# Performance work log

Measured on AMD Instinct MI355X. Metric: run time of the kernel, lower is better.

Reference implementation:

```python
import jax, jax.numpy as jnp
import numpy as np
from jax.scipy.special import logsumexp

EPS = 0.1
MAX_ITER = 10
THRESH = 0.1


def setup_inputs() -> dict:
    key = jax.random.key(0)
    k1, k2 = jax.random.split(key)
    N, P, D = 16, 1024, 64
    y = jax.random.normal(k1, (N, P, D), dtype=jnp.float32)
    x = jax.random.normal(k2, (N, P, D), dtype=jnp.float32)
    return {"y": y, "x": x}


def reference(y, x):
    # Cost matrix |x_i - y_j|^2 summed over feature dim: (N, P1, P2)
    C = jnp.sum(jnp.abs(x[:, :, None, :] - y[:, None, :, :]) ** 2, axis=-1)
    N, P1, P2 = C.shape
    mu = jnp.full((N, P1), 1.0 / P1, dtype=C.dtype)
    nu = jnp.full((N, P2), 1.0 / P2, dtype=C.dtype)

    def M(u, v):
        # (-C + u_i + v_j) / eps
        return (-C + u[:, :, None] + v[:, None, :]) / EPS

    def body(carry, _):
        u, v, done = carry
        u_new = EPS * (jnp.log(mu + 1e-8) - logsumexp(M(u, v), axis=-1)) + u
        v_new = EPS * (jnp.log(nu + 1e-8) - logsumexp(M(u_new, v), axis=-2)) + v
        err = jnp.abs(u_new - u).sum(-1).mean()
        # emulate torch's early break: freeze updates once converged
        u2 = jnp.where(done, u, u_new)
        v2 = jnp.where(done, v, v_new)
        done2 = done | (err < THRESH)
        return (u2, v2, done2), None

    u0 = jnp.zeros_like(mu)
    v0 = jnp.zeros_like(nu)
    (u, v, _), _ = jax.lax.scan(body, (u0, v0, jnp.array(False)), None, length=MAX_ITER)
    pi = jnp.exp(M(u, v))  # transport plan (N, P1, P2)
    return pi
```

## Files before the change

### kernel.cpp

```cpp
#include <hip/hip_runtime.h>
#include <math.h>

#define NB 16
#define PP 1024
#define DD 64
#define MAX_ITER 10
#define RCH 16
#define NCH (PP / RCH)
#define NBLK (NB * NCH)

constexpr float EPSV    = 0.1f;
constexpr float SCALE_G = 20.0f;
constexpr float LOG2E   = 1.44269504088896340736f;
constexpr float LOG_MU  = -6.93146156597137f;
constexpr float THRESHV = 0.1f;

typedef short bf16x8 __attribute__((ext_vector_type(8)));
typedef float f32x16 __attribute__((ext_vector_type(16)));

__device__ __forceinline__ unsigned short f2bf(float f) {
  unsigned int u = __float_as_uint(f);
  return (unsigned short)((u + 0x7FFFu + ((u >> 16) & 1u)) >> 16);
}
__device__ __forceinline__ float bf2f(unsigned short h) {
  return __uint_as_float(((unsigned int)h) << 16);
}

__global__ __launch_bounds__(256) void prep_kernel(
    const float* __restrict__ x, const float* __restrict__ y,
    unsigned short* __restrict__ xh, unsigned short* __restrict__ xl,
    unsigned short* __restrict__ yh, unsigned short* __restrict__ yl,
    float* __restrict__ nxs, float* __restrict__ nys)
{
  const int sel = blockIdx.x >> 9;
  const int row = (blockIdx.x & 511) * 32 + (threadIdx.x >> 3);
  const int q   = threadIdx.x & 7;

  const float* src = sel ? y : x;
  unsigned short* H = sel ? yh : xh;
  unsigned short* L = sel ? yl : xl;
  float* N          = sel ? nys : nxs;

  const float* p = src + (size_t)row * DD + q * 8;
  float4 v0 = *(const float4*)(p);
  float4 v1 = *(const float4*)(p + 4);

  float f[8] = {v0.x, v0.y, v0.z, v0.w, v1.x, v1.y, v1.z, v1.w};
  float nrm = 0.f;
  unsigned short hb[8], lb[8];
  #pragma unroll
  for (int k = 0; k < 8; ++k) {
    nrm = fmaf(f[k], f[k], nrm);
    unsigned short h = f2bf(f[k]);
    float res = f[k] - bf2f(h);
    hb[k] = h; lb[k] = f2bf(res);
  }
  nrm += __shfl_xor(nrm, 1);
  nrm += __shfl_xor(nrm, 2);
  nrm += __shfl_xor(nrm, 4);
  if (q == 0) N[row] = 10.0f * nrm;

  uint4 ho, lo;
  ho.x = hb[0] | ((unsigned)hb[1] << 16); ho.y = hb[2] | ((unsigned)hb[3] << 16);
  ho.z = hb[4] | ((unsigned)hb[5] << 16); ho.w = hb[6] | ((unsigned)hb[7] << 16);
  lo.x = lb[0] | ((unsigned)lb[1] << 16); lo.y = lb[2] | ((unsigned)lb[3] << 16);
  lo.z = lb[4] | ((unsigned)lb[5] << 16); lo.w = lb[6] | ((unsigned)lb[7] << 16);
  *(uint4*)(H + (size_t)row * DD + q * 8) = ho;
  *(uint4*)(L + (size_t)row * DD + q * 8) = lo;
}

__global__ __launch_bounds__(256) void compute_c_mfma(
    const unsigned short* __restrict__ xh, const unsigned short* __restrict__ xl,
    const float* __restrict__ nxs,
    const unsigned short* __restrict__ yh, const unsigned short* __restrict__ yl,
    const float* __restrict__ nys,
    float* __restrict__ Cs)
{
  const int n   = blockIdx.x >> 8;
  const int ib  = (blockIdx.x >> 4) & 15;
  const int jb  = blockIdx.x & 15;
  const int tid = threadIdx.x;
  const int l   = tid & 63;
  const int w   = tid >> 6;
  const int ih  = w & 1, jh = w >> 1;

  __shared__ float nxv[64];
  if (tid < 64) nxv[tid] = nxs[n * PP + ib * 64 + tid];
  __syncthreads();

  const int jg  = n * PP + jb * 64 + 32 * jh + (l & 31);
  const float nyv = nys[jg];

  const int ko = 8 * (l >> 5);
  const size_t xrow = ((size_t)(n * PP + ib * 64 + 32 * ih + (l & 31))) * DD;
  const size_t yrow = ((size_t)jg) * DD;

  bf16x8 Xh0 = *(const bf16x8*)(xh + xrow + 0 * 16 + ko);
  bf16x8 Xh1 = *(const bf16x8*)(xh + xrow + 1 * 16 + ko);
  bf16x8 Xh2 = *(const bf16x8*)(xh + xrow + 2 * 16 + ko);
  bf16x8 Xh3 = *(const bf16x8*)(xh + xrow + 3 * 16 + ko);
  bf16x8 Xl0 = *(const bf16x8*)(xl + xrow + 0 * 16 + ko);
  bf16x8 Xl1 = *(const bf16x8*)(xl + xrow + 1 * 16 + ko);
  bf16x8 Xl2 = *(const bf16x8*)(xl + xrow + 2 * 16 + ko);
  bf16x8 Xl3 = *(const bf16x8*)(xl + xrow + 3 * 16 + ko);
  bf16x8 Yh0 = *(const bf16x8*)(yh + yrow + 0 * 16 + ko);
  bf16x8 Yh1 = *(const bf16x8*)(yh + yrow + 1 * 16 + ko);
  bf16x8 Yh2 = *(const bf16x8*)(yh + yrow + 2 * 16 + ko);
  bf16x8 Yh3 = *(const bf16x8*)(yh + yrow + 3 * 16 + ko);
  bf16x8 Yl0 = *(const bf16x8*)(yl + yrow + 0 * 16 + ko);
  bf16x8 Yl1 = *(const bf16x8*)(yl + yrow + 1 * 16 + ko);
  bf16x8 Yl2 = *(const bf16x8*)(yl + yrow + 2 * 16 + ko);
  bf16x8 Yl3 = *(const bf16x8*)(yl + yrow + 3 * 16 + ko);

  f32x16 acc;
  #pragma unroll
  for (int z = 0; z < 16; ++z) acc[z] = 0.f;
  acc = __builtin_amdgcn_mfma_f32_32x32x16_bf16(Xh0, Yh0, acc, 0, 0, 0);
  acc = __builtin_amdgcn_mfma_f32_32x32x16_bf16(Xh1, Yh1, acc, 0, 0, 0);
  acc = __builtin_amdgcn_mfma_f32_32x32x16_bf16(Xh2, Yh2, acc, 0, 0, 0);
  acc = __builtin_amdgcn_mfma_f32_32x32x16_bf16(Xh3, Yh3, acc, 0, 0, 0);
  acc = __builtin_amdgcn_mfma_f32_32x32x16_bf16(Xh0, Yl0, acc, 0, 0, 0);
  acc = __builtin_amdgcn_mfma_f32_32x32x16_bf16(Xh1, Yl1, acc, 0, 0, 0);
  acc = __builtin_amdgcn_mfma_f32_32x32x16_bf16(Xh2, Yl2, acc, 0, 0, 0);
  acc = __builtin_amdgcn_mfma_f32_32x32x16_bf16(Xh3, Yl3, acc, 0, 0, 0);
  acc = __builtin_amdgcn_mfma_f32_32x32x16_bf16(Xl0, Yh0, acc, 0, 0, 0);
  acc = __builtin_amdgcn_mfma_f32_32x32x16_bf16(Xl1, Yh1, acc, 0, 0, 0);
  acc = __builtin_amdgcn_mfma_f32_32x32x16_bf16(Xl2, Yh2, acc, 0, 0, 0);
  acc = __builtin_amdgcn_mfma_f32_32x32x16_bf16(Xl3, Yh3, acc, 0, 0, 0);

  const int irb  = 32 * ih + 4 * (l >> 5);
  const int jcol = jb * 64 + 32 * jh + (l & 31);
  #pragma unroll
  for (int r = 0; r < 16; ++r) {
    const int irel = irb + (r & 3) + 8 * (r >> 2);
    const size_t off = ((size_t)(n * PP + ib * 64 + irel)) * PP + jcol;
    Cs[off] = nxv[irel] + nyv - SCALE_G * acc[r];
  }
}

__global__ __launch_bounds__(256, 4) void iter_fused(
    const float* __restrict__ Cs, float* __restrict__ aG, const float* __restrict__ bG,
    float* __restrict__ pm, float* __restrict__ ps, float* __restrict__ errBlk,
    const int* __restrict__ doneFlags, int it)
{
  if (it > 0 && doneFlags[it - 1]) return;

  const int n   = blockIdx.x >> 6;
  const int rc  = blockIdx.x & (NCH - 1);
  const int tid = threadIdx.x;

  __shared__ float bb[PP];
  __shared__ float aArr[RCH];
  __shared__ float dsum[RCH];

  if (it == 0) {
    *(float4*)&bb[tid * 4] = make_float4(0.f, 0.f, 0.f, 0.f);
  } else {
    *(float4*)&bb[tid * 4] = *(const float4*)(bG + n * PP + tid * 4);
  }
  __syncthreads();

  const int r0  = tid >> 4;
  const int k   = tid & 15;
  const int row = n * PP + rc * RCH + r0;
  const float* crow = Cs + (size_t)row * PP + 4 * k;

  float4 tv[16];
  #pragma unroll
  for (int j = 0; j < 16; ++j) {
    float4 c4 = *(const float4*)(crow + 64 * j);
    float4 b4 = *(const float4*)&bb[4 * k + 64 * j];
    tv[j] = make_float4(b4.x - c4.x, b4.y - c4.y, b4.z - c4.z, b4.w - c4.w);
  }
  float m = -INFINITY;
  #pragma unroll
  for (int j = 0; j < 16; ++j)
    m = fmaxf(m, fmaxf(fmaxf(tv[j].x, tv[j].y), fmaxf(tv[j].z, tv[j].w)));
  #pragma unroll
  for (int mask = 8; mask; mask >>= 1) m = fmaxf(m, __shfl_xor(m, mask));

  float s = 0.f;
  #pragma unroll
  for (int j = 0; j < 16; ++j) {
    s += exp2f((tv[j].x - m) * LOG2E) + exp2f((tv[j].y - m) * LOG2E)
       + exp2f((tv[j].z - m) * LOG2E) + exp2f((tv[j].w - m) * LOG2E);
  }
  #pragma unroll
  for (int mask = 8; mask; mask >>= 1) s += __shfl_xor(s, mask);

  if (k == 0) {
    float aOld = (it == 0) ? 0.f : aG[row];
    float an = LOG_MU - (m + logf(s));
    aG[row]  = an;
    aArr[r0] = an;
    dsum[r0] = fabsf(an - aOld);
  }
  __syncthreads();
  if (tid == 0) {
    float e = 0.f;
    #pragma unroll
    for (int r = 0; r < RCH; ++r) e += dsum[r];
    errBlk[blockIdx.x] = e;
  }

  const int c0 = tid * 4;
  const float* cb = Cs + ((size_t)(n * PP + rc * RCH)) * PP + c0;

  float m0 = -INFINITY, m1 = -INFINITY, m2 = -INFINITY, m3 = -INFINITY;
  #pragma unroll
  for (int r = 0; r < RCH; ++r) {
    float ar = aArr[r];
    float4 c4 = *(const float4*)(cb + (size_t)r * PP);
    m0 = fmaxf(m0, ar - c4.x);
    m1 = fmaxf(m1, ar - c4.y);
    m2 = fmaxf(m2, ar - c4.z);
    m3 = fmaxf(m3, ar - c4.w);
  }
  float s0 = 0.f, s1 = 0.f, s2 = 0.f, s3 = 0.f;
  #pragma unroll
  for (int r = 0; r < RCH; ++r) {
    float ar = aArr[r];
    float4 c4 = *(const float4*)(cb + (size_t)r * PP);
    s0 += exp2f((ar - c4.x - m0) * LOG2E);
    s1 += exp2f((ar - c4.y - m1) * LOG2E);
    s2 += exp2f((ar - c4.z - m2) * LOG2E);
    s3 += exp2f((ar - c4.w - m3) * LOG2E);
  }
  size_t off = ((size_t)(n * NCH + rc)) * PP + c0;
  *(float4*)(pm + off) = make_float4(m0, m1, m2, m3);
  *(float4*)(ps + off) = make_float4(s0, s1, s2, s3);
}

__global__ __launch_bounds__(256) void v_combine(
    const float* __restrict__ pm, const float* __restrict__ ps,
    float* __restrict__ bG, const float* __restrict__ errBlk,
    int* __restrict__ doneFlags, int it)
{
  if (it > 0 && doneFlags[it - 1]) {
    if (blockIdx.x == 0 && threadIdx.x == 0) doneFlags[it] = 1;
    return;
  }
  const int col = blockIdx.x * 256 + threadIdx.x;
  const int n = col >> 10, j = col & (PP - 1);
  const float* pmn = pm + (size_t)n * NCH * PP + j;
  const float* psn = ps + (size_t)n * NCH * PP + j;

  float m = -INFINITY, s = 0.f;
  #pragma unroll 8
  for (int c = 0; c < NCH; ++c) {
    float mc = pmn[(size_t)c * PP];
    float sc = psn[(size_t)c * PP];
    float mn = fmaxf(m, mc);
    s = fmaf(s, exp2f((m - mn) * LOG2E), sc * exp2f((mc - mn) * LOG2E));
    m = mn;
  }
  bG[col] = LOG_MU - (m + logf(s));

  if (blockIdx.x == 0) {
    __shared__ float red[4];
    float loc = 0.f;
    for (int t = threadIdx.x; t < NBLK; t += 256) loc += errBlk[t];
    #pragma unroll
    for (int off = 32; off > 0; off >>= 1) loc += __shfl_xor(loc, off);
    if ((threadIdx.x & 63) == 0) red[threadIdx.x >> 6] = loc;
    __syncthreads();
    if (threadIdx.x == 0) {
      float tot = red[0] + red[1] + red[2] + red[3];
      float err = tot * (EPSV / (float)NB);
      doneFlags[it] = (err < THRESHV) ? 1 : 0;
    }
  }
}

__global__ __launch_bounds__(256) void pi_kernel(
    float* __restrict__ Cs, const float* __restrict__ a, const float* __restrict__ b)
{
  const int lane = threadIdx.x & 63;
  const int row  = (blockIdx.x << 2) + (threadIdx.x >> 6);
  const int n    = row >> 10;
  const float ai = a[row];
  float* crow = Cs + (size_t)row * PP;
  const float* bn = b + n * PP;
  #pragma unroll
  for (int kk = 0; kk < 4; ++kk) {
    float4 c4 = *(const float4*)(crow + lane * 4 + kk * 256);
    float4 b4 = *(const float4*)(bn   + lane * 4 + kk * 256);
    float4 r;
    r.x = exp2f((ai + b4.x - c4.x) * LOG2E);
    r.y = exp2f((ai + b4.y - c4.y) * LOG2E);
    r.z = exp2f((ai + b4.z - c4.z) * LOG2E);
    r.w = exp2f((ai + b4.w - c4.w) * LOG2E);
    *(float4*)(crow + lane * 4 + kk * 256) = r;
  }
}

extern "C" void kernel_launch(void* const* d_in, const int* in_sizes, int n_in,
                              void* d_out, int out_size, void* d_ws, size_t ws_size,
                              hipStream_t stream)
{
  const float* y = (const float*)d_in[0];
  const float* x = (const float*)d_in[1];

  float* Cs = (float*)d_out;

  const size_t NE = (size_t)NB * PP * DD;
  unsigned short* xh = (unsigned short*)d_ws;
  unsigned short* xl = xh + NE;
  unsigned short* yh = xl + NE;
  unsigned short* yl = yh + NE;
  float* pm = (float*)d_ws;
  float* ps = pm + (size_t)NB * NCH * PP;

  float* tail   = (float*)((char*)d_ws + 4 * NE * sizeof(unsigned short));
  float* nxs    = tail;
  float* nys    = nxs + NB * PP;
  float* aGl    = nys + NB * PP;
  float* bGl    = aGl + NB * PP;
  float* errBlk = bGl + NB * PP;
  int*   doneFl = (int*)(errBlk + NBLK);

  prep_kernel<<<1024, 256, 0, stream>>>(x, y, xh, xl, yh, yl, nxs, nys);
  compute_c_mfma<<<4096, 256, 0, stream>>>(xh, xl, nxs, yh, yl, nys, Cs);
  for (int it = 0; it < MAX_ITER; ++it) {
    iter_fused<<<NBLK, 256, 0, stream>>>(Cs, aGl, bGl, pm, ps, errBlk, doneFl, it);
    v_combine<<<NB * PP / 256, 256, 0, stream>>>(pm, ps, bGl, errBlk, doneFl, it);
  }
  pi_kernel<<<NB * PP / 4, 256, 0, stream>>>(Cs, aGl, bGl);
}
```

Measured before the change: 378.6 us.

## Recompute cost tiles with MFMA in row logsumexp and use column-stripe v update

```diff
diff --git a/kernel.cpp b/kernel.cpp
--- a/kernel.cpp
+++ b/kernel.cpp
@@ -5,9 +5,6 @@
 #define PP 1024
 #define DD 64
 #define MAX_ITER 10
-#define RCH 16
-#define NCH (PP / RCH)
-#define NBLK (NB * NCH)
 
 constexpr float EPSV    = 0.1f;
 constexpr float SCALE_G = 20.0f;
@@ -138,136 +135,205 @@
   }
 }
 
-__global__ __launch_bounds__(256, 4) void iter_fused(
-    const float* __restrict__ Cs, float* __restrict__ aG, const float* __restrict__ bG,
-    float* __restrict__ pm, float* __restrict__ ps, float* __restrict__ errBlk,
-    const int* __restrict__ doneFlags, int it)
-{
-  if (it > 0 && doneFlags[it - 1]) return;
-
-  const int n   = blockIdx.x >> 6;
-  const int rc  = blockIdx.x & (NCH - 1);
-  const int tid = threadIdx.x;
-
-  __shared__ float bb[PP];
-  __shared__ float aArr[RCH];
-  __shared__ float dsum[RCH];
-
-  if (it == 0) {
-    *(float4*)&bb[tid * 4] = make_float4(0.f, 0.f, 0.f, 0.f);
-  } else {
-    *(float4*)&bb[tid * 4] = *(const float4*)(bG + n * PP + tid * 4);
-  }
-  __syncthreads();
-
-  const int r0  = tid >> 4;
-  const int k   = tid & 15;
-  const int row = n * PP + rc * RCH + r0;
-  const float* crow = Cs + (size_t)row * PP + 4 * k;
-
-  float4 tv[16];
-  #pragma unroll
-  for (int j = 0; j < 16; ++j) {
-    float4 c4 = *(const float4*)(crow + 64 * j);
-    float4 b4 = *(const float4*)&bb[4 * k + 64 * j];
-    tv[j] = make_float4(b4.x - c4.x, b4.y - c4.y, b4.z - c4.z, b4.w - c4.w);
-  }
+__global__ __launch_bounds__(256) void u_mfma(
+    const unsigned short* __restrict__ yh, const unsigned short* __restrict__ yl,
+    const float* __restrict__ nys,
+    const unsigned short* __restrict__ xh, const unsigned short* __restrict__ xl,
+    const float* __restrict__ nxs,
+    const float* __restrict__ bG, float* __restrict__ aG,
+    float* __restrict__ errBlk, const int* __restrict__ doneFl, int it)
+{
+  if (it > 0 && doneFl[it - 1]) return;
+
+  const int n     = blockIdx.x >> 5;
+  const int itile = blockIdx.x & 31;
+  const int tid   = threadIdx.x;
+  const int l     = tid & 63;
+  const int w     = tid >> 6;
+
+  __shared__ float bt[PP];
+  __shared__ float mred[4][32];
+  __shared__ float sred[4][32];
+
+  {
+    float4 nv = *(const float4*)(nys + n * PP + tid * 4);
+    float4 b4 = make_float4(0.f, 0.f, 0.f, 0.f);
+    if (it > 0) b4 = *(const float4*)(bG + n * PP + tid * 4);
+    bt[tid * 4 + 0] = b4.x - nv.x; bt[tid * 4 + 1] = b4.y - nv.y;
+    bt[tid * 4 + 2] = b4.z - nv.z; bt[tid * 4 + 3] = b4.w - nv.w;
+  }
+  __syncthreads();
+
+  const size_t brow = ((size_t)(n * PP + itile * 32 + (l & 31))) * DD;
+  const int ko = 8 * (l >> 5);
+  bf16x8 Bh0 = *(const bf16x8*)(xh + brow + 0 * 16 + ko);
+  bf16x8 Bh1 = *(const bf16x8*)(xh + brow + 1 * 16 + ko);
+  bf16x8 Bh2 = *(const bf16x8*)(xh + brow + 2 * 16 + ko);
+  bf16x8 Bh3 = *(const bf16x8*)(xh + brow + 3 * 16 + ko);
+  bf16x8 Bl0 = *(const bf16x8*)(xl + brow + 0 * 16 + ko);
+  bf16x8 Bl1 = *(const bf16x8*)(xl + brow + 1 * 16 + ko);
+  bf16x8 Bl2 = *(const bf16x8*)(xl + brow + 2 * 16 + ko);
+  bf16x8 Bl3 = *(const bf16x8*)(xl + brow + 3 * 16 + ko);
+
+  float M = -INFINITY;
+  for (int jt = 0; jt < 8; ++jt) {
+    const int jrow0 = w * 256 + jt * 32;
+    const size_t arow = ((size_t)(n * PP + jrow0 + (l & 31))) * DD;
+    bf16x8 Ah0 = *(const bf16x8*)(yh + arow + 0 * 16 + ko);
+    bf16x8 Ah1 = *(const bf16x8*)(yh + arow + 1 * 16 + ko);
+    bf16x8 Ah2 = *(const bf16x8*)(yh + arow + 2 * 16 + ko);
+    bf16x8 Ah3 = *(const bf16x8*)(yh + arow + 3 * 16 + ko);
+    bf16x8 Al0 = *(const bf16x8*)(yl + arow + 0 * 16 + ko);
+    bf16x8 Al1 = *(const bf16x8*)(yl + arow + 1 * 16 + ko);
+    bf16x8 Al2 = *(const bf16x8*)(yl + arow + 2 * 16 + ko);
+    bf16x8 Al3 = *(const bf16x8*)(yl + arow + 3 * 16 + ko);
+
+    f32x16 acc;
+    #pragma unroll
+    for (int z = 0; z < 16; ++z) acc[z] = 0.f;
+    acc = __builtin_amdgcn_mfma_f32_32x32x16_bf16(Ah0, Bh0, acc, 0, 0, 0);
+    acc = __builtin_amdgcn_mfma_f32_32x32x16_bf16(Ah1, Bh1, acc, 0, 0, 0);
+    acc = __builtin_amdgcn_mfma_f32_32x32x16_bf16(Ah2, Bh2, acc, 0, 0, 0);
+    acc = __builtin_amdgcn_mfma_f32_32x32x16_bf16(Ah3, Bh3, acc, 0, 0, 0);
+    acc = __builtin_amdgcn_mfma_f32_32x32x16_bf16(Ah0, Bl0, acc, 0, 0, 0);
+    acc = __builtin_amdgcn_mfma_f32_32x32x16_bf16(Ah1, Bl1, acc, 0, 0, 0);
+    acc = __builtin_amdgcn_mfma_f32_32x32x16_bf16(Ah2, Bl2, acc, 0, 0, 0);
+    acc = __builtin_amdgcn_mfma_f32_32x32x16_bf16(Ah3, Bl3, acc, 0, 0, 0);
+    acc = __builtin_amdgcn_mfma_f32_32x32x16_bf16(Al0, Bh0, acc, 0, 0, 0);
+    acc = __builtin_amdgcn_mfma_f32_32x32x16_bf16(Al1, Bh1, acc, 0, 0, 0);
+    acc = __builtin_amdgcn_mfma_f32_32x32x16_bf16(Al2, Bh2, acc, 0, 0, 0);
+    acc = __builtin_amdgcn_mfma_f32_32x32x16_bf16(Al3, Bh3, acc, 0, 0, 0);
+
+    const int jb = jrow0 + 4 * (l >> 5);
+    #pragma unroll
+    for (int r = 0; r < 16; ++r)
+      M = fmaxf(M, fmaf(SCALE_G, acc[r], bt[jb + (r & 3) + 8 * (r >> 2)]));
+  }
+  M = fmaxf(M, __shfl_xor(M, 32));
+  if (l < 32) mred[w][l] = M;
+  __syncthreads();
+
+  const int c = l & 31;
+  const float Mf = fmaxf(fmaxf(mred[0][c], mred[1][c]),
+                         fmaxf(mred[2][c], mred[3][c]));
+
+  float S = 0.f;
+  for (int jt = 0; jt < 8; ++jt) {
+    const int jrow0 = w * 256 + jt * 32;
+    const size_t arow = ((size_t)(n * PP + jrow0 + (l & 31))) * DD;
+    bf16x8 Ah0 = *(const bf16x8*)(yh + arow + 0 * 16 + ko);
+    bf16x8 Ah1 = *(const bf16x8*)(yh + arow + 1 * 16 + ko);
+    bf16x8 Ah2 = *(const bf16x8*)(yh + arow + 2 * 16 + ko);
+    bf16x8 Ah3 = *(const bf16x8*)(yh + arow + 3 * 16 + ko);
+    bf16x8 Al0 = *(const bf16x8*)(yl + arow + 0 * 16 + ko);
+    bf16x8 Al1 = *(const bf16x8*)(yl + arow + 1 * 16 + ko);
+    bf16x8 Al2 = *(const bf16x8*)(yl + arow + 2 * 16 + ko);
+    bf16x8 Al3 = *(const bf16x8*)(yl + arow + 3 * 16 + ko);
+
+    f32x16 acc;
+    #pragma unroll
+    for (int z = 0; z < 16; ++z) acc[z] = 0.f;
+    acc = __builtin_amdgcn_mfma_f32_32x32x16_bf16(Ah0, Bh0, acc, 0, 0, 0);
+    acc = __builtin_amdgcn_mfma_f32_32x32x16_bf16(Ah1, Bh1, acc, 0, 0, 0);
+    acc = __builtin_amdgcn_mfma_f32_32x32x16_bf16(Ah2, Bh2, acc, 0, 0, 0);
+    acc = __builtin_amdgcn_mfma_f32_32x32x16_bf16(Ah3, Bh3, acc, 0, 0, 0);
+    acc = __builtin_amdgcn_mfma_f32_32x32x16_bf16(Ah0, Bl0, acc, 0, 0, 0);
+    acc = __builtin_amdgcn_mfma_f32_32x32x16_bf16(Ah1, Bl1, acc, 0, 0, 0);
+    acc = __builtin_amdgcn_mfma_f32_32x32x16_bf16(Ah2, Bl2, acc, 0, 0, 0);
+    acc = __builtin_amdgcn_mfma_f32_32x32x16_bf16(Ah3, Bl3, acc, 0, 0, 0);
+    acc = __builtin_amdgcn_mfma_f32_32x32x16_bf16(Al0, Bh0, acc, 0, 0, 0);
+    acc = __builtin_amdgcn_mfma_f32_32x32x16_bf16(Al1, Bh1, acc, 0, 0, 0);
+    acc = __builtin_amdgcn_mfma_f32_32x32x16_bf16(Al2, Bh2, acc, 0, 0, 0);
+    acc = __builtin_amdgcn_mfma_f32_32x32x16_bf16(Al3, Bh3, acc, 0, 0, 0);
+
+    const int jb = jrow0 + 4 * (l >> 5);
+    #pragma unroll
+    for (int r = 0; r < 16; ++r)
+      S += exp2f((fmaf(SCALE_G, acc[r], bt[jb + (r & 3) + 8 * (r >> 2)]) - Mf) * LOG2E);
+  }
+  S += __shfl_xor(S, 32);
+  if (l < 32) sred[w][l] = S;
+  __syncthreads();
+
+  if (tid < 32) {
+    float Sf = sred[0][tid] + sred[1][tid] + sred[2][tid] + sred[3][tid];
+    float Mc = fmaxf(fmaxf(mred[0][tid], mred[1][tid]),
+                     fmaxf(mred[2][tid], mred[3][tid]));
+    const int gi = n * PP + itile * 32 + tid;
+    float newv = LOG_MU + nxs[gi] - (Mc + logf(Sf));
+    float aOld = (it == 0) ? 0.f : aG[gi];
+    aG[gi] = newv;
+    float dErr = fabsf(newv - aOld);
+    dErr += __shfl_xor(dErr, 1);
+    dErr += __shfl_xor(dErr, 2);
+    dErr += __shfl_xor(dErr, 4);
+    dErr += __shfl_xor(dErr, 8);
+    dErr += __shfl_xor(dErr, 16);
+    if (tid == 0) errBlk[blockIdx.x] = dErr;
+  }
+}
+
+__global__ __launch_bounds__(256) void v_stripe(
+    const float* __restrict__ Cs, const float* __restrict__ aG,
+    float* __restrict__ bG, const float* __restrict__ errBlk,
+    int* __restrict__ doneFl, int it)
+{
+  if (it > 0 && doneFl[it - 1]) {
+    if (blockIdx.x == 0 && threadIdx.x == 0) doneFl[it] = 1;
+    return;
+  }
+  __shared__ float as[PP];
+  __shared__ float red[8][33];
+
+  const int n  = blockIdx.x >> 5;
+  const int jt = blockIdx.x & 31;
+  const float* an = aG + n * PP;
+  for (int t = threadIdx.x; t < PP; t += 256) as[t] = an[t];
+  __syncthreads();
+
+  const int tx = threadIdx.x & 31;
+  const int ty = threadIdx.x >> 5;
+  const float* cb = Cs + (size_t)n * PP * PP + jt * 32 + tx;
+
   float m = -INFINITY;
-  #pragma unroll
-  for (int j = 0; j < 16; ++j)
-    m = fmaxf(m, fmaxf(fmaxf(tv[j].x, tv[j].y), fmaxf(tv[j].z, tv[j].w)));
-  #pragma unroll
-  for (int mask = 8; mask; mask >>= 1) m = fmaxf(m, __shfl_xor(m, mask));
+  #pragma unroll 8
+  for (int i = ty; i < PP; i += 8)
+    m = fmaxf(m, as[i] - cb[(size_t)i * PP]);
+
+  red[ty][tx] = m;
+  __syncthreads();
+  if (ty == 0) {
+    #pragma unroll
+    for (int k = 1; k < 8; ++k) m = fmaxf(m, red[k][tx]);
+    red[0][tx] = m;
+  }
+  __syncthreads();
+  m = red[0][tx];
 
   float s = 0.f;
-  #pragma unroll
-  for (int j = 0; j < 16; ++j) {
-    s += exp2f((tv[j].x - m) * LOG2E) + exp2f((tv[j].y - m) * LOG2E)
-       + exp2f((tv[j].z - m) * LOG2E) + exp2f((tv[j].w - m) * LOG2E);
-  }
-  #pragma unroll
-  for (int mask = 8; mask; mask >>= 1) s += __shfl_xor(s, mask);
-
-  if (k == 0) {
-    float aOld = (it == 0) ? 0.f : aG[row];
-    float an = LOG_MU - (m + logf(s));
-    aG[row]  = an;
-    aArr[r0] = an;
-    dsum[r0] = fabsf(an - aOld);
-  }
-  __syncthreads();
-  if (tid == 0) {
-    float e = 0.f;
-    #pragma unroll
-    for (int r = 0; r < RCH; ++r) e += dsum[r];
-    errBlk[blockIdx.x] = e;
-  }
-
-  const int c0 = tid * 4;
-  const float* cb = Cs + ((size_t)(n * PP + rc * RCH)) * PP + c0;
-
-  float m0 = -INFINITY, m1 = -INFINITY, m2 = -INFINITY, m3 = -INFINITY;
-  #pragma unroll
-  for (int r = 0; r < RCH; ++r) {
-    float ar = aArr[r];
-    float4 c4 = *(const float4*)(cb + (size_t)r * PP);
-    m0 = fmaxf(m0, ar - c4.x);
-    m1 = fmaxf(m1, ar - c4.y);
-    m2 = fmaxf(m2, ar - c4.z);
-    m3 = fmaxf(m3, ar - c4.w);
-  }
-  float s0 = 0.f, s1 = 0.f, s2 = 0.f, s3 = 0.f;
-  #pragma unroll
-  for (int r = 0; r < RCH; ++r) {
-    float ar = aArr[r];
-    float4 c4 = *(const float4*)(cb + (size_t)r * PP);
-    s0 += exp2f((ar - c4.x - m0) * LOG2E);
-    s1 += exp2f((ar - c4.y - m1) * LOG2E);
-    s2 += exp2f((ar - c4.z - m2) * LOG2E);
-    s3 += exp2f((ar - c4.w - m3) * LOG2E);
-  }
-  size_t off = ((size_t)(n * NCH + rc)) * PP + c0;
-  *(float4*)(pm + off) = make_float4(m0, m1, m2, m3);
-  *(float4*)(ps + off) = make_float4(s0, s1, s2, s3);
-}
-
-__global__ __launch_bounds__(256) void v_combine(
-    const float* __restrict__ pm, const float* __restrict__ ps,
-    float* __restrict__ bG, const float* __restrict__ errBlk,
-    int* __restrict__ doneFlags, int it)
-{
-  if (it > 0 && doneFlags[it - 1]) {
-    if (blockIdx.x == 0 && threadIdx.x == 0) doneFlags[it] = 1;
-    return;
-  }
-  const int col = blockIdx.x * 256 + threadIdx.x;
-  const int n = col >> 10, j = col & (PP - 1);
-  const float* pmn = pm + (size_t)n * NCH * PP + j;
-  const float* psn = ps + (size_t)n * NCH * PP + j;
-
-  float m = -INFINITY, s = 0.f;
   #pragma unroll 8
-  for (int c = 0; c < NCH; ++c) {
-    float mc = pmn[(size_t)c * PP];
-    float sc = psn[(size_t)c * PP];
-    float mn = fmaxf(m, mc);
-    s = fmaf(s, exp2f((m - mn) * LOG2E), sc * exp2f((mc - mn) * LOG2E));
-    m = mn;
-  }
-  bG[col] = LOG_MU - (m + logf(s));
+  for (int i = ty; i < PP; i += 8)
+    s += exp2f((as[i] - cb[(size_t)i * PP] - m) * LOG2E);
+
+  __syncthreads();
+  red[ty][tx] = s;
+  __syncthreads();
+  if (ty == 0) {
+    #pragma unroll
+    for (int k = 1; k < 8; ++k) s += red[k][tx];
+    bG[n * PP + jt * 32 + tx] = LOG_MU - (m + logf(s));
+  }
 
   if (blockIdx.x == 0) {
-    __shared__ float red[4];
-    float loc = 0.f;
-    for (int t = threadIdx.x; t < NBLK; t += 256) loc += errBlk[t];
-    #pragma unroll
-    for (int off = 32; off > 0; off >>= 1) loc += __shfl_xor(loc, off);
-    if ((threadIdx.x & 63) == 0) red[threadIdx.x >> 6] = loc;
+    __syncthreads();
+    float loc = errBlk[threadIdx.x] + errBlk[threadIdx.x + 256];
+    #pragma unroll
+    for (int mk = 32; mk; mk >>= 1) loc += __shfl_xor(loc, mk);
+    if ((threadIdx.x & 63) == 0) red[0][threadIdx.x >> 6] = loc;
     __syncthreads();
     if (threadIdx.x == 0) {
-      float tot = red[0] + red[1] + red[2] + red[3];
-      float err = tot * (EPSV / (float)NB);
-      doneFlags[it] = (err < THRESHV) ? 1 : 0;
+      float tot = red[0][0] + red[0][1] + red[0][2] + red[0][3];
+      doneFl[it] = (tot * (EPSV / (float)NB) < THRESHV) ? 1 : 0;
     }
   }
 }
@@ -308,22 +374,19 @@
   unsigned short* xl = xh + NE;
   unsigned short* yh = xl + NE;
   unsigned short* yl = yh + NE;
-  float* pm = (float*)d_ws;
-  float* ps = pm + (size_t)NB * NCH * PP;
-
-  float* tail   = (float*)((char*)d_ws + 4 * NE * sizeof(unsigned short));
-  float* nxs    = tail;
+  float* nxs    = (float*)(yl + NE);
   float* nys    = nxs + NB * PP;
-  float* aGl    = nys + NB * PP;
-  float* bGl    = aGl + NB * PP;
-  float* errBlk = bGl + NB * PP;
-  int*   doneFl = (int*)(errBlk + NBLK);
+  float* aG     = nys + NB * PP;
+  float* bG     = aG + NB * PP;
+  float* errBlk = bG + NB * PP;
+  int*   doneFl = (int*)(errBlk + 512);
 
   prep_kernel<<<1024, 256, 0, stream>>>(x, y, xh, xl, yh, yl, nxs, nys);
   compute_c_mfma<<<4096, 256, 0, stream>>>(xh, xl, nxs, yh, yl, nys, Cs);
   for (int it = 0; it < MAX_ITER; ++it) {
-    iter_fused<<<NBLK, 256, 0, stream>>>(Cs, aGl, bGl, pm, ps, errBlk, doneFl, it);
-    v_combine<<<NB * PP / 256, 256, 0, stream>>>(pm, ps, bGl, errBlk, doneFl, it);
-  }
-  pi_kernel<<<NB * PP / 4, 256, 0, stream>>>(Cs, aGl, bGl);
-}
+    u_mfma<<<512, 256, 0, stream>>>(yh, yl, nys, xh, xl, nxs,
+                                    bG, aG, errBlk, doneFl, it);
+    v_stripe<<<512, 256, 0, stream>>>(Cs, aG, bG, errBlk, doneFl, it);
+  }
+  pi_kernel<<<NB * PP / 4, 256, 0, stream>>>(Cs, aG, bG);
+}
```

New measurement: 788.7 us. +108.3%, slower.

## Recompute cost tiles with MFMA inside Sinkhorn iterations instead of streaming C

Applied to the files above, without the earlier changes.

```diff
diff --git a/kernel.cpp b/kernel.cpp
--- a/kernel.cpp
+++ b/kernel.cpp
@@ -5,9 +5,7 @@
 #define PP 1024
 #define DD 64
 #define MAX_ITER 10
-#define RCH 16
-#define NCH (PP / RCH)
-#define NBLK (NB * NCH)
+#define CH (NB * PP)
 
 constexpr float EPSV    = 0.1f;
 constexpr float SCALE_G = 20.0f;
@@ -67,6 +65,293 @@
   lo.z = lb[4] | ((unsigned)lb[5] << 16); lo.w = lb[6] | ((unsigned)lb[7] << 16);
   *(uint4*)(H + (size_t)row * DD + q * 8) = ho;
   *(uint4*)(L + (size_t)row * DD + q * 8) = lo;
+}
+
+__global__ __launch_bounds__(256) void u_half(
+    const unsigned short* __restrict__ Ahp, const unsigned short* __restrict__ Alp,
+    const unsigned short* __restrict__ Bhp, const unsigned short* __restrict__ Blp,
+    const float* __restrict__ nA,
+    const float* __restrict__ pmIn, const float* __restrict__ psIn,
+    float* __restrict__ pmOut, float* __restrict__ psOut,
+    const float* __restrict__ errBlk, int it)
+{
+  const int tid = threadIdx.x;
+  if (it > 0) {
+    const float* eb = errBlk + ((it - 1) & 1) * NB;
+    float tot = 0.f;
+    #pragma unroll
+    for (int k = 0; k < NB; ++k) tot += eb[k];
+    if (tot * (EPSV / (float)NB) < THRESHV) return;
+  }
+  const int n     = blockIdx.x >> 6;
+  const int rem   = blockIdx.x & 63;
+  const int otile = rem >> 1;
+  const int rc    = rem & 1;
+  const int l     = tid & 63;
+  const int w     = tid >> 6;
+
+  __shared__ float bias[PP];
+  __shared__ float mred[4][32];
+  __shared__ float sred[4][32];
+
+  {
+    const int e0 = tid * 4;
+    if (it == 0) {
+      float4 nv = *(const float4*)(nA + n * PP + e0);
+      bias[e0+0] = -nv.x; bias[e0+1] = -nv.y; bias[e0+2] = -nv.z; bias[e0+3] = -nv.w;
+    } else {
+      float4 m0 = *(const float4*)(pmIn + 0 * CH + n * PP + e0);
+      float4 m1 = *(const float4*)(pmIn + 1 * CH + n * PP + e0);
+      float4 s0 = *(const float4*)(psIn + 0 * CH + n * PP + e0);
+      float4 s1 = *(const float4*)(psIn + 1 * CH + n * PP + e0);
+      float mm, ss;
+      mm = fmaxf(m0.x, m1.x);
+      ss = s0.x * exp2f((m0.x - mm) * LOG2E) + s1.x * exp2f((m1.x - mm) * LOG2E);
+      bias[e0+0] = LOG_MU - (mm + logf(ss));
+      mm = fmaxf(m0.y, m1.y);
+      ss = s0.y * exp2f((m0.y - mm) * LOG2E) + s1.y * exp2f((m1.y - mm) * LOG2E);
+      bias[e0+1] = LOG_MU - (mm + logf(ss));
+      mm = fmaxf(m0.z, m1.z);
+      ss = s0.z * exp2f((m0.z - mm) * LOG2E) + s1.z * exp2f((m1.z - mm) * LOG2E);
+      bias[e0+2] = LOG_MU - (mm + logf(ss));
+      mm = fmaxf(m0.w, m1.w);
+      ss = s0.w * exp2f((m0.w - mm) * LOG2E) + s1.w * exp2f((m1.w - mm) * LOG2E);
+      bias[e0+3] = LOG_MU - (mm + logf(ss));
+    }
+  }
+  __syncthreads();
+
+  const size_t brow = ((size_t)(n * PP + otile * 32 + (l & 31))) * DD;
+  const int ko = 8 * (l >> 5);
+  bf16x8 Bh[4], Bl[4];
+  #pragma unroll
+  for (int q = 0; q < 4; ++q) {
+    Bh[q] = *(const bf16x8*)(Bhp + brow + q * 16 + ko);
+    Bl[q] = *(const bf16x8*)(Blp + brow + q * 16 + ko);
+  }
+
+  float M = -INFINITY;
+  for (int jt = 0; jt < 4; ++jt) {
+    const int jrow0 = rc * 512 + w * 128 + jt * 32;
+    const size_t arow = ((size_t)(n * PP + jrow0 + (l & 31))) * DD;
+    f32x16 a0, a1, a2;
+    #pragma unroll
+    for (int z = 0; z < 16; ++z) { a0[z] = 0.f; a1[z] = 0.f; a2[z] = 0.f; }
+    #pragma unroll
+    for (int q = 0; q < 4; ++q) {
+      bf16x8 Ah = *(const bf16x8*)(Ahp + arow + q * 16 + ko);
+      bf16x8 Al = *(const bf16x8*)(Alp + arow + q * 16 + ko);
+      a0 = __builtin_amdgcn_mfma_f32_32x32x16_bf16(Ah, Bh[q], a0, 0, 0, 0);
+      a1 = __builtin_amdgcn_mfma_f32_32x32x16_bf16(Ah, Bl[q], a1, 0, 0, 0);
+      a2 = __builtin_amdgcn_mfma_f32_32x32x16_bf16(Al, Bh[q], a2, 0, 0, 0);
+    }
+    const int jb = jrow0 + 4 * (l >> 5);
+    #pragma unroll
+    for (int r = 0; r < 16; ++r)
+      M = fmaxf(M, fmaf(SCALE_G, a0[r] + a1[r] + a2[r], bias[jb + (r & 3) + 8 * (r >> 2)]));
+  }
+  M = fmaxf(M, __shfl_xor(M, 32));
+  if (l < 32) mred[w][l] = M;
+  __syncthreads();
+  const int c = l & 31;
+  const float Mf = fmaxf(fmaxf(mred[0][c], mred[1][c]), fmaxf(mred[2][c], mred[3][c]));
+
+  float S = 0.f;
+  for (int jt = 0; jt < 4; ++jt) {
+    const int jrow0 = rc * 512 + w * 128 + jt * 32;
+    const size_t arow = ((size_t)(n * PP + jrow0 + (l & 31))) * DD;
+    f32x16 a0, a1, a2;
+    #pragma unroll
+    for (int z = 0; z < 16; ++z) { a0[z] = 0.f; a1[z] = 0.f; a2[z] = 0.f; }
+    #pragma unroll
+    for (int q = 0; q < 4; ++q) {
+      bf16x8 Ah = *(const bf16x8*)(Ahp + arow + q * 16 + ko);
+      bf16x8 Al = *(const bf16x8*)(Alp + arow + q * 16 + ko);
+      a0 = __builtin_amdgcn_mfma_f32_32x32x16_bf16(Ah, Bh[q], a0, 0, 0, 0);
+      a1 = __builtin_amdgcn_mfma_f32_32x32x16_bf16(Ah, Bl[q], a1, 0, 0, 0);
+      a2 = __builtin_amdgcn_mfma_f32_32x32x16_bf16(Al, Bh[q], a2, 0, 0, 0);
+    }
+    const int jb = jrow0 + 4 * (l >> 5);
+    #pragma unroll
+    for (int r = 0; r < 16; ++r)
+      S += exp2f((fmaf(SCALE_G, a0[r] + a1[r] + a2[r], bias[jb + (r & 3) + 8 * (r >> 2)]) - Mf) * LOG2E);
+  }
+  S += __shfl_xor(S, 32);
+  if (l < 32) sred[w][l] = S;
+  __syncthreads();
+
+  if (tid < 32) {
+    float Sf = sred[0][tid] + sred[1][tid] + sred[2][tid] + sred[3][tid];
+    float Mc = fmaxf(fmaxf(mred[0][tid], mred[1][tid]), fmaxf(mred[2][tid], mred[3][tid]));
+    const int gi = n * PP + otile * 32 + tid;
+    pmOut[rc * CH + gi] = Mc;
+    psOut[rc * CH + gi] = Sf;
+  }
+}
+
+__global__ __launch_bounds__(256) void v_half(
+    const unsigned short* __restrict__ Ahp, const unsigned short* __restrict__ Alp,
+    const unsigned short* __restrict__ Bhp, const unsigned short* __restrict__ Blp,
+    const float* __restrict__ nxs,
+    const float* __restrict__ pmIn, const float* __restrict__ psIn,
+    float* __restrict__ pmOut, float* __restrict__ psOut,
+    float* __restrict__ atPrev, float* __restrict__ errBlk, int it)
+{
+  const int tid = threadIdx.x;
+  const int n   = blockIdx.x >> 6;
+  const int rem = blockIdx.x & 63;
+  if (it > 0) {
+    const float* eb = errBlk + ((it - 1) & 1) * NB;
+    float tot = 0.f;
+    #pragma unroll
+    for (int k = 0; k < NB; ++k) tot += eb[k];
+    if (tot * (EPSV / (float)NB) < THRESHV) {
+      if (rem == 0 && tid == 0)
+        errBlk[(it & 1) * NB + n] = errBlk[((it - 1) & 1) * NB + n];
+      return;
+    }
+  }
+  const int otile = rem >> 1;
+  const int rc    = rem & 1;
+  const int l     = tid & 63;
+  const int w     = tid >> 6;
+
+  __shared__ float bias[PP];
+  __shared__ float mred[4][32];
+  __shared__ float sred[4][32];
+  __shared__ float red4[4];
+
+  float dsumT = 0.f;
+  {
+    const int e0 = tid * 4;
+    float4 m0 = *(const float4*)(pmIn + 0 * CH + n * PP + e0);
+    float4 m1 = *(const float4*)(pmIn + 1 * CH + n * PP + e0);
+    float4 s0 = *(const float4*)(psIn + 0 * CH + n * PP + e0);
+    float4 s1 = *(const float4*)(psIn + 1 * CH + n * PP + e0);
+    float at4[4];
+    float mm, ss;
+    mm = fmaxf(m0.x, m1.x);
+    ss = s0.x * exp2f((m0.x - mm) * LOG2E) + s1.x * exp2f((m1.x - mm) * LOG2E);
+    at4[0] = LOG_MU - (mm + logf(ss));
+    mm = fmaxf(m0.y, m1.y);
+    ss = s0.y * exp2f((m0.y - mm) * LOG2E) + s1.y * exp2f((m1.y - mm) * LOG2E);
+    at4[1] = LOG_MU - (mm + logf(ss));
+    mm = fmaxf(m0.z, m1.z);
+    ss = s0.z * exp2f((m0.z - mm) * LOG2E) + s1.z * exp2f((m1.z - mm) * LOG2E);
+    at4[2] = LOG_MU - (mm + logf(ss));
+    mm = fmaxf(m0.w, m1.w);
+    ss = s0.w * exp2f((m0.w - mm) * LOG2E) + s1.w * exp2f((m1.w - mm) * LOG2E);
+    at4[3] = LOG_MU - (mm + logf(ss));
+    bias[e0+0] = at4[0]; bias[e0+1] = at4[1]; bias[e0+2] = at4[2]; bias[e0+3] = at4[3];
+    if (rem == 0) {
+      if (it == 0) {
+        float4 nx = *(const float4*)(nxs + n * PP + e0);
+        dsumT = fabsf(at4[0] + nx.x) + fabsf(at4[1] + nx.y)
+              + fabsf(at4[2] + nx.z) + fabsf(at4[3] + nx.w);
+      } else {
+        float4 ap = *(const float4*)(atPrev + n * PP + e0);
+        dsumT = fabsf(at4[0] - ap.x) + fabsf(at4[1] - ap.y)
+              + fabsf(at4[2] - ap.z) + fabsf(at4[3] - ap.w);
+      }
+      *(float4*)(atPrev + n * PP + e0) = make_float4(at4[0], at4[1], at4[2], at4[3]);
+    }
+  }
+  __syncthreads();
+
+  const size_t brow = ((size_t)(n * PP + otile * 32 + (l & 31))) * DD;
+  const int ko = 8 * (l >> 5);
+  bf16x8 Bh[4], Bl[4];
+  #pragma unroll
+  for (int q = 0; q < 4; ++q) {
+    Bh[q] = *(const bf16x8*)(Bhp + brow + q * 16 + ko);
+    Bl[q] = *(const bf16x8*)(Blp + brow + q * 16 + ko);
+  }
+
+  float M = -INFINITY;
+  for (int jt = 0; jt < 4; ++jt) {
+    const int jrow0 = rc * 512 + w * 128 + jt * 32;
+    const size_t arow = ((size_t)(n * PP + jrow0 + (l & 31))) * DD;
+    f32x16 a0, a1, a2;
+    #pragma unroll
+    for (int z = 0; z < 16; ++z) { a0[z] = 0.f; a1[z] = 0.f; a2[z] = 0.f; }
+    #pragma unroll
+    for (int q = 0; q < 4; ++q) {
+      bf16x8 Ah = *(const bf16x8*)(Ahp + arow + q * 16 + ko);
+      bf16x8 Al = *(const bf16x8*)(Alp + arow + q * 16 + ko);
+      a0 = __builtin_amdgcn_mfma_f32_32x32x16_bf16(Ah, Bh[q], a0, 0, 0, 0);
+      a1 = __builtin_amdgcn_mfma_f32_32x32x16_bf16(Ah, Bl[q], a1, 0, 0, 0);
+      a2 = __builtin_amdgcn_mfma_f32_32x32x16_bf16(Al, Bh[q], a2, 0, 0, 0);
+    }
+    const int jb = jrow0 + 4 * (l >> 5);
+    #pragma unroll
+    for (int r = 0; r < 16; ++r)
+      M = fmaxf(M, fmaf(SCALE_G, a0[r] + a1[r] + a2[r], bias[jb + (r & 3) + 8 * (r >> 2)]));
+  }
+  M = fmaxf(M, __shfl_xor(M, 32));
+  if (l < 32) mred[w][l] = M;
+  __syncthreads();
+  const int c = l & 31;
+  const float Mf = fmaxf(fmaxf(mred[0][c], mred[1][c]), fmaxf(mred[2][c], mred[3][c]));
+
+  float S = 0.f;
+  for (int jt = 0; jt < 4; ++jt) {
+    const int jrow0 = rc * 512 + w * 128 + jt * 32;
+    const size_t arow = ((size_t)(n * PP + jrow0 + (l & 31))) * DD;
+    f32x16 a0, a1, a2;
+    #pragma unroll
+    for (int z = 0; z < 16; ++z) { a0[z] = 0.f; a1[z] = 0.f; a2[z] = 0.f; }
+    #pragma unroll
+    for (int q = 0; q < 4; ++q) {
+      bf16x8 Ah = *(const bf16x8*)(Ahp + arow + q * 16 + ko);
+      bf16x8 Al = *(const bf16x8*)(Alp + arow + q * 16 + ko);
+      a0 = __builtin_amdgcn_mfma_f32_32x32x16_bf16(Ah, Bh[q], a0, 0, 0, 0);
+      a1 = __builtin_amdgcn_mfma_f32_32x32x16_bf16(Ah, Bl[q], a1, 0, 0, 0);
+      a2 = __builtin_amdgcn_mfma_f32_32x32x16_bf16(Al, Bh[q], a2, 0, 0, 0);
+    }
+    const int jb = jrow0 + 4 * (l >> 5);
+    #pragma unroll
+    for (int r = 0; r < 16; ++r)
+      S += exp2f((fmaf(SCALE_G, a0[r] + a1[r] + a2[r], bias[jb + (r & 3) + 8 * (r >> 2)]) - Mf) * LOG2E);
+  }
+  S += __shfl_xor(S, 32);
+  if (l < 32) sred[w][l] = S;
+  __syncthreads();
+
+  if (tid < 32) {
+    float Sf = sred[0][tid] + sred[1][tid] + sred[2][tid] + sred[3][tid];
+    float Mc = fmaxf(fmaxf(mred[0][tid], mred[1][tid]), fmaxf(mred[2][tid], mred[3][tid]));
+    const int gi = n * PP + otile * 32 + tid;
+    pmOut[rc * CH + gi] = Mc;
+    psOut[rc * CH + gi] = Sf;
+  }
+
+  if (rem == 0) {
+    #pragma unroll
+    for (int off = 32; off; off >>= 1) dsumT += __shfl_xor(dsumT, off);
+    if (l == 0) red4[w] = dsumT;
+  }
+  __syncthreads();
+  if (rem == 0 && tid == 0)
+    errBlk[(it & 1) * NB + n] = red4[0] + red4[1] + red4[2] + red4[3];
+}
+
+__global__ __launch_bounds__(256) void finalize_duals(
+    const float* __restrict__ pmU, const float* __restrict__ psU,
+    const float* __restrict__ pmV, const float* __restrict__ psV,
+    const float* __restrict__ nxs, const float* __restrict__ nys,
+    float* __restrict__ aG, float* __restrict__ bG)
+{
+  const int gi = blockIdx.x * 256 + threadIdx.x;
+  float m0 = pmU[gi], m1 = pmU[CH + gi];
+  float s0 = psU[gi], s1 = psU[CH + gi];
+  float mm = fmaxf(m0, m1);
+  float ss = s0 * exp2f((m0 - mm) * LOG2E) + s1 * exp2f((m1 - mm) * LOG2E);
+  aG[gi] = LOG_MU + nxs[gi] - (mm + logf(ss));
+  m0 = pmV[gi]; m1 = pmV[CH + gi];
+  s0 = psV[gi]; s1 = psV[CH + gi];
+  mm = fmaxf(m0, m1);
+  ss = s0 * exp2f((m0 - mm) * LOG2E) + s1 * exp2f((m1 - mm) * LOG2E);
+  bG[gi] = LOG_MU + nys[gi] - (mm + logf(ss));
 }
 
 __global__ __launch_bounds__(256) void compute_c_mfma(
@@ -138,140 +423,6 @@
   }
 }
 
-__global__ __launch_bounds__(256, 4) void iter_fused(
-    const float* __restrict__ Cs, float* __restrict__ aG, const float* __restrict__ bG,
-    float* __restrict__ pm, float* __restrict__ ps, float* __restrict__ errBlk,
-    const int* __restrict__ doneFlags, int it)
-{
-  if (it > 0 && doneFlags[it - 1]) return;
-
-  const int n   = blockIdx.x >> 6;
-  const int rc  = blockIdx.x & (NCH - 1);
-  const int tid = threadIdx.x;
-
-  __shared__ float bb[PP];
-  __shared__ float aArr[RCH];
-  __shared__ float dsum[RCH];
-
-  if (it == 0) {
-    *(float4*)&bb[tid * 4] = make_float4(0.f, 0.f, 0.f, 0.f);
-  } else {
-    *(float4*)&bb[tid * 4] = *(const float4*)(bG + n * PP + tid * 4);
-  }
-  __syncthreads();
-
-  const int r0  = tid >> 4;
-  const int k   = tid & 15;
-  const int row = n * PP + rc * RCH + r0;
-  const float* crow = Cs + (size_t)row * PP + 4 * k;
-
-  float4 tv[16];
-  #pragma unroll
-  for (int j = 0; j < 16; ++j) {
-    float4 c4 = *(const float4*)(crow + 64 * j);
-    float4 b4 = *(const float4*)&bb[4 * k + 64 * j];
-    tv[j] = make_float4(b4.x - c4.x, b4.y - c4.y, b4.z - c4.z, b4.w - c4.w);
-  }
-  float m = -INFINITY;
-  #pragma unroll
-  for (int j = 0; j < 16; ++j)
-    m = fmaxf(m, fmaxf(fmaxf(tv[j].x, tv[j].y), fmaxf(tv[j].z, tv[j].w)));
-  #pragma unroll
-  for (int mask = 8; mask; mask >>= 1) m = fmaxf(m, __shfl_xor(m, mask));
-
-  float s = 0.f;
-  #pragma unroll
-  for (int j = 0; j < 16; ++j) {
-    s += exp2f((tv[j].x - m) * LOG2E) + exp2f((tv[j].y - m) * LOG2E)
-       + exp2f((tv[j].z - m) * LOG2E) + exp2f((tv[j].w - m) * LOG2E);
-  }
-  #pragma unroll
-  for (int mask = 8; mask; mask >>= 1) s += __shfl_xor(s, mask);
-
-  if (k == 0) {
-    float aOld = (it == 0) ? 0.f : aG[row];
-    float an = LOG_MU - (m + logf(s));
-    aG[row]  = an;
-    aArr[r0] = an;
-    dsum[r0] = fabsf(an - aOld);
-  }
-  __syncthreads();
-  if (tid == 0) {
-    float e = 0.f;
-    #pragma unroll
-    for (int r = 0; r < RCH; ++r) e += dsum[r];
-    errBlk[blockIdx.x] = e;
-  }
-
-  const int c0 = tid * 4;
-  const float* cb = Cs + ((size_t)(n * PP + rc * RCH)) * PP + c0;
-
-  float m0 = -INFINITY, m1 = -INFINITY, m2 = -INFINITY, m3 = -INFINITY;
-  #pragma unroll
-  for (int r = 0; r < RCH; ++r) {
-    float ar = aArr[r];
-    float4 c4 = *(const float4*)(cb + (size_t)r * PP);
-    m0 = fmaxf(m0, ar - c4.x);
-    m1 = fmaxf(m1, ar - c4.y);
-    m2 = fmaxf(m2, ar - c4.z);
-    m3 = fmaxf(m3, ar - c4.w);
-  }
-  float s0 = 0.f, s1 = 0.f, s2 = 0.f, s3 = 0.f;
-  #pragma unroll
-  for (int r = 0; r < RCH; ++r) {
-    float ar = aArr[r];
-    float4 c4 = *(const float4*)(cb + (size_t)r * PP);
-    s0 += exp2f((ar - c4.x - m0) * LOG2E);
-    s1 += exp2f((ar - c4.y - m1) * LOG2E);
-    s2 += exp2f((ar - c4.z - m2) * LOG2E);
-    s3 += exp2f((ar - c4.w - m3) * LOG2E);
-  }
-  size_t off = ((size_t)(n * NCH + rc)) * PP + c0;
-  *(float4*)(pm + off) = make_float4(m0, m1, m2, m3);
-  *(float4*)(ps + off) = make_float4(s0, s1, s2, s3);
-}
-
-__global__ __launch_bounds__(256) void v_combine(
-    const float* __restrict__ pm, const float* __restrict__ ps,
-    float* __restrict__ bG, const float* __restrict__ errBlk,
-    int* __restrict__ doneFlags, int it)
-{
-  if (it > 0 && doneFlags[it - 1]) {
-    if (blockIdx.x == 0 && threadIdx.x == 0) doneFlags[it] = 1;
-    return;
-  }
-  const int col = blockIdx.x * 256 + threadIdx.x;
-  const int n = col >> 10, j = col & (PP - 1);
-  const float* pmn = pm + (size_t)n * NCH * PP + j;
-  const float* psn = ps + (size_t)n * NCH * PP + j;
-
-  float m = -INFINITY, s = 0.f;
-  #pragma unroll 8
-  for (int c = 0; c < NCH; ++c) {
-    float mc = pmn[(size_t)c * PP];
-    float sc = psn[(size_t)c * PP];
-    float mn = fmaxf(m, mc);
-    s = fmaf(s, exp2f((m - mn) * LOG2E), sc * exp2f((mc - mn) * LOG2E));
-    m = mn;
-  }
-  bG[col] = LOG_MU - (m + logf(s));
-
-  if (blockIdx.x == 0) {
-    __shared__ float red[4];
-    float loc = 0.f;
-    for (int t = threadIdx.x; t < NBLK; t += 256) loc += errBlk[t];
-    #pragma unroll
-    for (int off = 32; off > 0; off >>= 1) loc += __shfl_xor(loc, off);
-    if ((threadIdx.x & 63) == 0) red[threadIdx.x >> 6] = loc;
-    __syncthreads();
-    if (threadIdx.x == 0) {
-      float tot = red[0] + red[1] + red[2] + red[3];
-      float err = tot * (EPSV / (float)NB);
-      doneFlags[it] = (err < THRESHV) ? 1 : 0;
-    }
-  }
-}
-
 __global__ __launch_bounds__(256) void pi_kernel(
     float* __restrict__ Cs, const float* __restrict__ a, const float* __restrict__ b)
 {
@@ -308,22 +459,25 @@
   unsigned short* xl = xh + NE;
   unsigned short* yh = xl + NE;
   unsigned short* yl = yh + NE;
-  float* pm = (float*)d_ws;
-  float* ps = pm + (size_t)NB * NCH * PP;
-
-  float* tail   = (float*)((char*)d_ws + 4 * NE * sizeof(unsigned short));
-  float* nxs    = tail;
-  float* nys    = nxs + NB * PP;
-  float* aGl    = nys + NB * PP;
-  float* bGl    = aGl + NB * PP;
-  float* errBlk = bGl + NB * PP;
-  int*   doneFl = (int*)(errBlk + NBLK);
+  float* nxs    = (float*)(yl + NE);
+  float* nys    = nxs + CH;
+  float* pmU    = nys + CH;
+  float* psU    = pmU + 2 * CH;
+  float* pmV    = psU + 2 * CH;
+  float* psV    = pmV + 2 * CH;
+  float* atPrev = psV + 2 * CH;
+  float* aG     = atPrev + CH;
+  float* bG     = aG + CH;
+  float* errBlk = bG + CH;
 
   prep_kernel<<<1024, 256, 0, stream>>>(x, y, xh, xl, yh, yl, nxs, nys);
+  for (int it = 0; it < MAX_ITER; ++it) {
+    u_half<<<1024, 256, 0, stream>>>(yh, yl, xh, xl, nys,
+                                     pmV, psV, pmU, psU, errBlk, it);
+    v_half<<<1024, 256, 0, stream>>>(xh, xl, yh, yl, nxs,
+                                     pmU, psU, pmV, psV, atPrev, errBlk, it);
+  }
+  finalize_duals<<<64, 256, 0, stream>>>(pmU, psU, pmV, psV, nxs, nys, aG, bG);
   compute_c_mfma<<<4096, 256, 0, stream>>>(xh, xl, nxs, yh, yl, nys, Cs);
-  for (int it = 0; it < MAX_ITER; ++it) {
-    iter_fused<<<NBLK, 256, 0, stream>>>(Cs, aGl, bGl, pm, ps, errBlk, doneFl, it);
-    v_combine<<<NB * PP / 256, 256, 0, stream>>>(pm, ps, bGl, errBlk, doneFl, it);
-  }
-  pi_kernel<<<NB * PP / 4, 256, 0, stream>>>(Cs, aGl, bGl);
-}
+  pi_kernel<<<NB * PP / 4, 256, 0, stream>>>(Cs, aG, bG);
+}
```

Result: slower. 820.0 us (+116.6%).
